# Optimization experiments

Measured on AMD Instinct MI355X. Metric: run time of the kernel, lower is better.

## Reference

```python
import jax, jax.numpy as jnp
import numpy as np

B, D, T, K = 8, 512, 2048, 8192


def setup_inputs() -> dict:
    key = jax.random.key(0)
    k1, k2 = jax.random.split(key)
    latents = jax.random.normal(k1, (B, D, T), dtype=jnp.float32)
    # nn.Embedding weight initialized uniform(-1/K, 1/K)
    embedding = jax.random.uniform(k2, (K, D), dtype=jnp.float32,
                                   minval=-1.0 / K, maxval=1.0 / K)
    return {"latents": latents, "embedding": embedding}


def reference(latents, embedding):
    # latents: [B, D, T] -> [B, T, D]
    x = jnp.transpose(latents, (0, 2, 1))
    # argmin over squared distance == argmin over cdist(p=2), so output matches torch.
    x_sq = jnp.sum(x * x, axis=-1, keepdims=True)            # [B, T, 1]
    e_sq = jnp.sum(embedding * embedding, axis=-1)           # [K]
    cross = jnp.einsum("btd,kd->btk", x, embedding)          # [B, T, K]
    dist2 = x_sq - 2.0 * cross + e_sq                        # [B, T, K]
    encoding_inds = jnp.argmin(dist2, axis=-1)               # [B, T] int
    quantized = embedding[encoding_inds]                     # [B, T, D]
    return jnp.transpose(quantized, (0, 2, 1))               # [B, D, T]
```

## Files before the change

kernel.cpp:

```cpp
#include <hip/hip_runtime.h>
#include <hip/hip_bf16.h>
#include <cstdint>

constexpr int Dv = 512;
constexpr int Tv = 2048;
constexpr int Kv = 8192;
constexpr int BT = 16384;

constexpr int BQ = 128;
constexpr int BK = 128;
constexpr int BD = 32;
constexpr int NKC = Kv / BK;
constexpr int BPQ = 6;
constexpr int NBLK = (BT / BQ) * BPQ;

__global__ void vq_xsq(const float* __restrict__ lat, float* __restrict__ xsq) {
    int q = blockIdx.x * 256 + threadIdx.x;
    int b = q >> 11, t = q & 2047;
    const float* p = lat + (size_t)b * Dv * Tv + t;
    float a = 0.f;
    #pragma unroll 8
    for (int d = 0; d < Dv; ++d) {
        float v = p[(size_t)d * Tv];
        a = fmaf(v, v, a);
    }
    xsq[q] = a;
}

__global__ void vq_esq(const float* __restrict__ emb, float* __restrict__ esq) {
    int gid = blockIdx.x * 256 + threadIdx.x;
    int k = gid >> 6;
    int l = threadIdx.x & 63;
    const float* p = emb + (size_t)k * Dv + l;
    float a = 0.f;
    #pragma unroll
    for (int i = 0; i < 8; ++i) {
        float v = p[i * 64];
        a = fmaf(v, v, a);
    }
    #pragma unroll
    for (int off = 32; off; off >>= 1) a += __shfl_down(a, off, 64);
    if (l == 0) esq[k] = a;
}

__global__ void vq_init(unsigned long long* __restrict__ keys) {
    int q = blockIdx.x * 256 + threadIdx.x;
    keys[q] = 0xFFFFFFFFFFFFFFFFull;
}

__global__ __launch_bounds__(256, 3) void vq_main(
        const float* __restrict__ lat, const float* __restrict__ emb,
        const float* __restrict__ xsq, const float* __restrict__ esq,
        unsigned long long* __restrict__ keys) {
    __shared__ float Xs[BD][BQ];
    __shared__ float Es[BD][BK];

    const int tid = threadIdx.x;
    const int bid = blockIdx.x;
    const int qb  = bid / BPQ;
    const int sub = bid - qb * BPQ;
    const int q0 = qb * BQ;
    const int b  = q0 >> 11;
    const int t0 = q0 & 2047;
    const int cnt = (sub < 4) ? 11 : 10;
    const int kc0 = (sub < 4) ? sub * 11 : 44 + (sub - 4) * 10;

    const int tx = (tid & 7) | (((tid >> 6) & 1) << 3);
    const int ty = ((tid >> 3) & 7) | (((tid >> 7) & 1) << 3);

    const int sq   = tid & 31;
    const int srow = tid >> 5;
    const int dq   = tid & 7;
    const int ekk  = tid >> 3;
    const int fsw  = dq << 2;

    float best[8];
    int   bidx[8];
    float xs[8];
    #pragma unroll
    for (int i = 0; i < 8; ++i) {
        best[i] = 3.4e38f;
        bidx[i] = 0x7fffffff;
        xs[i] = xsq[q0 + ty * 8 + i];
    }

    const float* latb = lat + (size_t)b * Dv * Tv + t0;
    float* const esw = &Es[0][0];

    for (int kc = kc0; kc < kc0 + cnt; ++kc) {
        const int k0 = kc * BK;
        float c[8][8];
        #pragma unroll
        for (int i = 0; i < 8; ++i)
            #pragma unroll
            for (int j = 0; j < 8; ++j) c[i][j] = 0.f;

        for (int dc = 0; dc < Dv / BD; ++dc) {
            const int d0 = dc * BD;
            __syncthreads();
            #pragma unroll
            for (int i = 0; i < 4; ++i) {
                int dd = srow + i * 8;
                float4 v = *(const float4*)(latb + (size_t)(d0 + dd) * Tv + sq * 4);
                *(float4*)&Xs[dd][sq * 4] = v;
            }
            #pragma unroll
            for (int i = 0; i < 4; ++i) {
                int kk = ekk + i * 32;
                float4 v = *(const float4*)(emb + (size_t)(k0 + kk) * Dv + d0 + dq * 4);
                int ksw = kk ^ fsw;
                esw[(dq * 4 + 0) * BK + ksw] = v.x;
                esw[(dq * 4 + 1) * BK + ksw] = v.y;
                esw[(dq * 4 + 2) * BK + ksw] = v.z;
                esw[(dq * 4 + 3) * BK + ksw] = v.w;
            }
            __syncthreads();

            #pragma unroll 4
            for (int dd = 0; dd < BD; ++dd) {
                const int g = (dd >> 2) << 2;
                const float4 xa = *(const float4*)&Xs[dd][ty * 8];
                const float4 xb = *(const float4*)&Xs[dd][ty * 8 + 4];
                const float4 ea = *(const float4*)&esw[dd * BK + ((tx * 8) ^ g)];
                const float4 eb = *(const float4*)&esw[dd * BK + ((tx * 8 + 4) ^ g)];
                #define VQ_ROW(i, XV)                       \
                    c[i][0] = fmaf(XV, ea.x, c[i][0]);      \
                    c[i][1] = fmaf(XV, ea.y, c[i][1]);      \
                    c[i][2] = fmaf(XV, ea.z, c[i][2]);      \
                    c[i][3] = fmaf(XV, ea.w, c[i][3]);      \
                    c[i][4] = fmaf(XV, eb.x, c[i][4]);      \
                    c[i][5] = fmaf(XV, eb.y, c[i][5]);      \
                    c[i][6] = fmaf(XV, eb.z, c[i][6]);      \
                    c[i][7] = fmaf(XV, eb.w, c[i][7]);
                VQ_ROW(0, xa.x) VQ_ROW(1, xa.y) VQ_ROW(2, xa.z) VQ_ROW(3, xa.w)
                VQ_ROW(4, xb.x) VQ_ROW(5, xb.y) VQ_ROW(6, xb.z) VQ_ROW(7, xb.w)
                #undef VQ_ROW
            }
        }

        float es8[8];
        #pragma unroll
        for (int j = 0; j < 8; ++j) es8[j] = esq[k0 + tx * 8 + j];
        #pragma unroll
        for (int i = 0; i < 8; ++i)
            #pragma unroll
            for (int j = 0; j < 8; ++j) {
                float dist = fmaf(-2.0f, c[i][j], xs[i]) + es8[j];
                int kk = k0 + tx * 8 + j;
                if (dist < best[i]) { best[i] = dist; bidx[i] = kk; }
            }
    }

    __syncthreads();
    float* redv = &Xs[0][0];
    int*   redi = (int*)&Es[0][0];
    #pragma unroll
    for (int i = 0; i < 8; ++i) {
        redv[(ty * 16 + tx) * 8 + i] = best[i];
        redi[(ty * 16 + tx) * 8 + i] = bidx[i];
    }
    __syncthreads();
    if (tid < 128) {
        int yy = tid >> 3, ii = tid & 7;
        float bv = 3.4e38f;
        int bi = 0x7fffffff;
        #pragma unroll
        for (int t = 0; t < 16; ++t) {
            float v = redv[(yy * 16 + t) * 8 + ii];
            int  ix = redi[(yy * 16 + t) * 8 + ii];
            if (v < bv || (v == bv && ix < bi)) { bv = v; bi = ix; }
        }
        int q = q0 + yy * 8 + ii;
        unsigned long long key =
            ((unsigned long long)__float_as_uint(bv) << 32) | (unsigned int)bi;
        atomicMin(&keys[q], key);
    }
}

__global__ void vq_gather(const float* __restrict__ emb,
                          const unsigned long long* __restrict__ keys,
                          float* __restrict__ out) {
    int blk = blockIdx.x;
    int tid = threadIdx.x;
    int tl = tid & 63, dg = tid >> 6;
    int q = blk * 64 + tl;
    int b = q >> 11, t = q & 2047;
    int idx = (int)(keys[q] & 0xFFFFFFFFull);
    const float* er = emb + (size_t)idx * Dv + dg * 128;
    float* ob = out + ((size_t)b * Dv + dg * 128) * Tv + t;
    #pragma unroll 8
    for (int i = 0; i < 128; ++i) ob[(size_t)i * Tv] = er[i];
}

extern "C" void kernel_launch(void* const* d_in, const int* in_sizes, int n_in,
                              void* d_out, int out_size, void* d_ws, size_t ws_size,
                              hipStream_t stream) {
    (void)in_sizes; (void)n_in; (void)out_size; (void)ws_size;
    const float* lat = (const float*)d_in[0];
    const float* emb = (const float*)d_in[1];
    float* out = (float*)d_out;

    char* ws = (char*)d_ws;
    float* xsq = (float*)(ws);
    float* esq = (float*)(ws + (64 << 10));
    unsigned long long* keys =
        (unsigned long long*)(ws + (96 << 10));

    vq_init <<<BT / 256, 256, 0, stream>>>(keys);
    vq_xsq  <<<BT / 256, 256, 0, stream>>>(lat, xsq);
    vq_esq  <<<Kv / 4,   256, 0, stream>>>(emb, esq);
    vq_main <<<NBLK, 256, 0, stream>>>(lat, emb, xsq, esq, keys);
    vq_gather<<<BT / 64, 256, 0, stream>>>(emb, keys, out);
}
```

Before: 1.874 ms.

## Add bf16 MFMA candidate filter with exact fp32 rescoring of near-minimum codes

Converts the latents (transposed) and the codebook to bf16 and computes all distances with MFMA 16x16x32 bf16 instructions. Each query keeps a running minimum, and codes within an error margin derived from the query's L1 norm are written to a candidate list. A rescore kernel then recomputes only those candidates exactly in fp32 and takes the argmin. This replaces the full fp32 FMA GEMM with tensor-core work plus a sparse exact pass, at the cost of relying on a heuristic margin, atomic contention on the candidate counter, a fixed candidate cap, and a fallback to the exact kernel when the workspace is too small.

Result: slower. 4.549 ms (+142.8%).

```diff
diff --git a/kernel.cpp b/kernel.cpp
--- a/kernel.cpp
+++ b/kernel.cpp
@@ -6,25 +6,30 @@
 constexpr int Tv = 2048;
 constexpr int Kv = 8192;
 constexpr int BT = 16384;
-
-constexpr int BQ = 128;
-constexpr int BK = 128;
-constexpr int BD = 32;
-constexpr int NKC = Kv / BK;
-constexpr int BPQ = 6;
-constexpr int NBLK = (BT / BQ) * BPQ;
-
-__global__ void vq_xsq(const float* __restrict__ lat, float* __restrict__ xsq) {
+constexpr unsigned CAP = 4u << 20;
+
+typedef __bf16 v8bf __attribute__((ext_vector_type(8)));
+typedef float  f32x4 __attribute__((ext_vector_type(4)));
+typedef unsigned long long u64;
+
+__device__ __forceinline__ float margin2(float S) {
+    return 3.9e-6f * S + 3.2e-4f;
+}
+
+__global__ void vq_xsq(const float* __restrict__ lat, float* __restrict__ xsq,
+                       float* __restrict__ Ssum) {
     int q = blockIdx.x * 256 + threadIdx.x;
     int b = q >> 11, t = q & 2047;
     const float* p = lat + (size_t)b * Dv * Tv + t;
-    float a = 0.f;
+    float a = 0.f, s = 0.f;
     #pragma unroll 8
     for (int d = 0; d < Dv; ++d) {
         float v = p[(size_t)d * Tv];
         a = fmaf(v, v, a);
+        s = s + fabsf(v);
     }
     xsq[q] = a;
+    Ssum[q] = s;
 }
 
 __global__ void vq_esq(const float* __restrict__ emb, float* __restrict__ esq) {
@@ -43,60 +48,245 @@
     if (l == 0) esq[k] = a;
 }
 
-__global__ void vq_init(unsigned long long* __restrict__ keys) {
+__global__ void vq_init_keys(u64* __restrict__ keys) {
     int q = blockIdx.x * 256 + threadIdx.x;
     keys[q] = 0xFFFFFFFFFFFFFFFFull;
 }
-
-__global__ __launch_bounds__(256, 3) void vq_main(
+__global__ void vq_init_aux(unsigned* __restrict__ qmin, unsigned* __restrict__ ctr) {
+    int q = blockIdx.x * 256 + threadIdx.x;
+    qmin[q] = 0xFFFFFFFFu;
+    if (q == 0) *ctr = 0u;
+}
+
+__global__ void vq_cvt_e(const float* __restrict__ emb, ushort* __restrict__ Ebf) {
+    int i = blockIdx.x * 256 + threadIdx.x;
+    const float4 v0 = *(const float4*)(emb + (size_t)i * 8);
+    const float4 v1 = *(const float4*)(emb + (size_t)i * 8 + 4);
+    ushort o[8];
+    float f[8] = {v0.x, v0.y, v0.z, v0.w, v1.x, v1.y, v1.z, v1.w};
+    #pragma unroll
+    for (int j = 0; j < 8; ++j) {
+        __hip_bfloat16 h = __float2bfloat16(f[j]);
+        o[j] = *(ushort*)&h;
+    }
+    *(uint4*)(Ebf + (size_t)i * 8) = *(uint4*)o;
+}
+
+__global__ void vq_cvt_x(const float* __restrict__ lat, ushort* __restrict__ Xbf) {
+    __shared__ float Xs[64][65];
+    int blk = blockIdx.x;
+    int tb = blk & 31, db = (blk >> 5) & 7, b = blk >> 8;
+    int d0 = db * 64, t0 = tb * 64;
+    int tid = threadIdx.x;
+    #pragma unroll
+    for (int i = 0; i < 4; ++i) {
+        int r = (tid >> 4) + i * 16;
+        int c = (tid & 15) * 4;
+        float4 v = *(const float4*)(lat + ((size_t)(b * Dv + d0 + r)) * Tv + t0 + c);
+        Xs[r][c] = v.x; Xs[r][c + 1] = v.y; Xs[r][c + 2] = v.z; Xs[r][c + 3] = v.w;
+    }
+    __syncthreads();
+    int tt = tid >> 2, dg = tid & 3;
+    int q = b * Tv + t0 + tt;
+    #pragma unroll
+    for (int i = 0; i < 2; ++i) {
+        ushort o[8];
+        #pragma unroll
+        for (int j = 0; j < 8; ++j) {
+            __hip_bfloat16 h = __float2bfloat16(Xs[dg * 16 + i * 8 + j][tt]);
+            o[j] = *(ushort*)&h;
+        }
+        *(uint4*)(Xbf + (size_t)q * Dv + d0 + dg * 16 + i * 8) = *(uint4*)o;
+    }
+}
+
+__global__ void vq_mfma(const ushort* __restrict__ Xbf, const ushort* __restrict__ Ebf,
+                        const float* __restrict__ es, const float* __restrict__ Ssum,
+                        unsigned* __restrict__ qmin, u64* __restrict__ cand,
+                        unsigned* __restrict__ ctr) {
+    __shared__ ushort Abuf[128 * 40];
+    __shared__ ushort Bbuf[128 * 40];
+    __shared__ unsigned tminl[128];
+    __shared__ float thrl[128];
+
+    const int tid = threadIdx.x;
+    const int bid = blockIdx.x;
+    const int q0 = (bid >> 6) * 128;
+    const int k0 = (bid & 63) * 128;
+    const int w = tid >> 6, l = tid & 63;
+    const int wr = w >> 1, wc = w & 1;
+
+    const int ar = tid >> 1, ah = tid & 1;
+
+    f32x4 acc[4][4] = {};
+
+    const ushort* Ag = Xbf + (size_t)(q0 + ar) * Dv + ah * 16;
+    const ushort* Bg = Ebf + (size_t)(k0 + ar) * Dv + ah * 16;
+
+    uint4 pa0 = *(const uint4*)(Ag);
+    uint4 pa1 = *(const uint4*)(Ag + 8);
+    uint4 pb0 = *(const uint4*)(Bg);
+    uint4 pb1 = *(const uint4*)(Bg + 8);
+
+    for (int s = 0; s < 16; ++s) {
+        __syncthreads();
+        *(uint4*)&Abuf[ar * 40 + ah * 16] = pa0;
+        *(uint4*)&Abuf[ar * 40 + ah * 16 + 8] = pa1;
+        *(uint4*)&Bbuf[ar * 40 + ah * 16] = pb0;
+        *(uint4*)&Bbuf[ar * 40 + ah * 16 + 8] = pb1;
+        __syncthreads();
+        if (s < 15) {
+            int d0 = (s + 1) * 32;
+            pa0 = *(const uint4*)(Ag + d0);
+            pa1 = *(const uint4*)(Ag + d0 + 8);
+            pb0 = *(const uint4*)(Bg + d0);
+            pb1 = *(const uint4*)(Bg + d0 + 8);
+        }
+        v8bf afr[4], bfc[4];
+        #pragma unroll
+        for (int f = 0; f < 4; ++f) {
+            int arow = wr * 64 + f * 16 + (l & 15);
+            afr[f] = __builtin_bit_cast(v8bf, *(const uint4*)&Abuf[arow * 40 + (l >> 4) * 8]);
+            int brow = wc * 64 + f * 16 + (l & 15);
+            bfc[f] = __builtin_bit_cast(v8bf, *(const uint4*)&Bbuf[brow * 40 + (l >> 4) * 8]);
+        }
+        #pragma unroll
+        for (int fr = 0; fr < 4; ++fr)
+            #pragma unroll
+            for (int fc = 0; fc < 4; ++fc)
+                acc[fr][fc] = __builtin_amdgcn_mfma_f32_16x16x32_bf16(
+                    afr[fr], bfc[fc], acc[fr][fc], 0, 0, 0);
+    }
+
+    if (tid < 128) tminl[tid] = 0xFFFFFFFFu;
+    __syncthreads();
+
+    float esv[4];
+    #pragma unroll
+    for (int fc = 0; fc < 4; ++fc) esv[fc] = es[k0 + wc * 64 + fc * 16 + (l & 15)];
+
+    #pragma unroll
+    for (int fr = 0; fr < 4; ++fr) {
+        float rmin[4] = {3.4e38f, 3.4e38f, 3.4e38f, 3.4e38f};
+        #pragma unroll
+        for (int fc = 0; fc < 4; ++fc)
+            #pragma unroll
+            for (int v = 0; v < 4; ++v) {
+                float kf = fmaf(-2.0f, acc[fr][fc][v], esv[fc]) + 1.0f;
+                rmin[v] = fminf(rmin[v], kf);
+            }
+        #pragma unroll
+        for (int v = 0; v < 4; ++v) {
+            float m = rmin[v];
+            m = fminf(m, __shfl_xor(m, 1, 64));
+            m = fminf(m, __shfl_xor(m, 2, 64));
+            m = fminf(m, __shfl_xor(m, 4, 64));
+            m = fminf(m, __shfl_xor(m, 8, 64));
+            if ((l & 15) == 0)
+                atomicMin(&tminl[wr * 64 + fr * 16 + (l >> 4) * 4 + v], __float_as_uint(m));
+        }
+    }
+    __syncthreads();
+    if (tid < 128) {
+        unsigned tm = tminl[tid];
+        unsigned old = atomicMin(&qmin[q0 + tid], tm);
+        unsigned eff = old < tm ? old : tm;
+        thrl[tid] = __uint_as_float(eff) + margin2(Ssum[q0 + tid]);
+    }
+    __syncthreads();
+    #pragma unroll
+    for (int fr = 0; fr < 4; ++fr)
+        #pragma unroll
+        for (int fc = 0; fc < 4; ++fc)
+            #pragma unroll
+            for (int v = 0; v < 4; ++v) {
+                float kf = fmaf(-2.0f, acc[fr][fc][v], esv[fc]) + 1.0f;
+                int qloc = wr * 64 + fr * 16 + (l >> 4) * 4 + v;
+                if (kf <= thrl[qloc]) {
+                    unsigned id = atomicAdd(ctr, 1u);
+                    if (id < CAP) {
+                        int kk = k0 + wc * 64 + fc * 16 + (l & 15);
+                        cand[id] = ((u64)__float_as_uint(kf) << 32)
+                                 | ((u64)(unsigned)(q0 + qloc) << 13) | (unsigned)kk;
+                    }
+                }
+            }
+}
+
+__global__ void vq_rescore(const float* __restrict__ lat, const float* __restrict__ emb,
+                           const float* __restrict__ xs, const float* __restrict__ es,
+                           const float* __restrict__ Ssum,
+                           const unsigned* __restrict__ qmin,
+                           const u64* __restrict__ cand, const unsigned* __restrict__ ctr,
+                           u64* __restrict__ keys) {
+    unsigned total = *ctr;
+    if (total > CAP) total = CAP;
+    for (unsigned i = blockIdx.x * 256 + threadIdx.x; i < total; i += 4096 * 256) {
+        u64 c = cand[i];
+        float kf = __uint_as_float((unsigned)(c >> 32));
+        int q = (int)((c >> 13) & 16383u);
+        int k = (int)(c & 8191u);
+        float thr = __uint_as_float(qmin[q]) + margin2(Ssum[q]);
+        if (kf > thr) continue;
+        int b = q >> 11, t = q & 2047;
+        const float* xr = lat + (size_t)b * Dv * Tv + t;
+        const float* er = emb + (size_t)k * Dv;
+        float cc = 0.f;
+        #pragma unroll 8
+        for (int d = 0; d < Dv; ++d)
+            cc = fmaf(xr[(size_t)d * Tv], er[d], cc);
+        float dist = fmaf(-2.0f, cc, xs[q]) + es[k];
+        u64 key = ((u64)__float_as_uint(dist) << 32) | (unsigned)k;
+        atomicMin(&keys[q], key);
+    }
+}
+
+__global__ void vq_gather(const float* __restrict__ emb, const u64* __restrict__ keys,
+                          float* __restrict__ out) {
+    int blk = blockIdx.x;
+    int tid = threadIdx.x;
+    int tl = tid & 63, dg = tid >> 6;
+    int q = blk * 64 + tl;
+    int b = q >> 11, t = q & 2047;
+    int idx = (int)(keys[q] & 0xFFFFFFFFull);
+    const float* er = emb + (size_t)idx * Dv + dg * 128;
+    float* ob = out + ((size_t)b * Dv + dg * 128) * Tv + t;
+    #pragma unroll 8
+    for (int i = 0; i < 128; ++i) ob[(size_t)i * Tv] = er[i];
+}
+
+constexpr int FBQ = 128, FBK = 128, FBD = 32, FBPQ = 6;
+__global__ __launch_bounds__(256, 3) void vq_main_exact(
         const float* __restrict__ lat, const float* __restrict__ emb,
         const float* __restrict__ xsq, const float* __restrict__ esq,
-        unsigned long long* __restrict__ keys) {
-    __shared__ float Xs[BD][BQ];
-    __shared__ float Es[BD][BK];
-
-    const int tid = threadIdx.x;
-    const int bid = blockIdx.x;
-    const int qb  = bid / BPQ;
-    const int sub = bid - qb * BPQ;
-    const int q0 = qb * BQ;
-    const int b  = q0 >> 11;
-    const int t0 = q0 & 2047;
+        u64* __restrict__ keys) {
+    __shared__ float Xs[FBD][FBQ];
+    __shared__ float Es[FBD][FBK];
+    const int tid = threadIdx.x, bid = blockIdx.x;
+    const int qb = bid / FBPQ, sub = bid - qb * FBPQ;
+    const int q0 = qb * FBQ, b = q0 >> 11, t0 = q0 & 2047;
     const int cnt = (sub < 4) ? 11 : 10;
     const int kc0 = (sub < 4) ? sub * 11 : 44 + (sub - 4) * 10;
-
     const int tx = (tid & 7) | (((tid >> 6) & 1) << 3);
     const int ty = ((tid >> 3) & 7) | (((tid >> 7) & 1) << 3);
-
-    const int sq   = tid & 31;
-    const int srow = tid >> 5;
-    const int dq   = tid & 7;
-    const int ekk  = tid >> 3;
-    const int fsw  = dq << 2;
-
-    float best[8];
-    int   bidx[8];
-    float xs[8];
+    const int sq = tid & 31, srow = tid >> 5;
+    const int dq = tid & 7, ekk = tid >> 3, fsw = dq << 2;
+    float best[8]; int bidx[8]; float xsv[8];
     #pragma unroll
     for (int i = 0; i < 8; ++i) {
-        best[i] = 3.4e38f;
-        bidx[i] = 0x7fffffff;
-        xs[i] = xsq[q0 + ty * 8 + i];
-    }
-
+        best[i] = 3.4e38f; bidx[i] = 0x7fffffff; xsv[i] = xsq[q0 + ty * 8 + i];
+    }
     const float* latb = lat + (size_t)b * Dv * Tv + t0;
     float* const esw = &Es[0][0];
-
     for (int kc = kc0; kc < kc0 + cnt; ++kc) {
-        const int k0 = kc * BK;
+        const int k0 = kc * FBK;
         float c[8][8];
         #pragma unroll
         for (int i = 0; i < 8; ++i)
             #pragma unroll
             for (int j = 0; j < 8; ++j) c[i][j] = 0.f;
-
-        for (int dc = 0; dc < Dv / BD; ++dc) {
-            const int d0 = dc * BD;
+        for (int dc = 0; dc < Dv / FBD; ++dc) {
+            const int d0 = dc * FBD;
             __syncthreads();
             #pragma unroll
             for (int i = 0; i < 4; ++i) {
@@ -109,20 +299,19 @@
                 int kk = ekk + i * 32;
                 float4 v = *(const float4*)(emb + (size_t)(k0 + kk) * Dv + d0 + dq * 4);
                 int ksw = kk ^ fsw;
-                esw[(dq * 4 + 0) * BK + ksw] = v.x;
-                esw[(dq * 4 + 1) * BK + ksw] = v.y;
-                esw[(dq * 4 + 2) * BK + ksw] = v.z;
-                esw[(dq * 4 + 3) * BK + ksw] = v.w;
+                esw[(dq * 4 + 0) * FBK + ksw] = v.x;
+                esw[(dq * 4 + 1) * FBK + ksw] = v.y;
+                esw[(dq * 4 + 2) * FBK + ksw] = v.z;
+                esw[(dq * 4 + 3) * FBK + ksw] = v.w;
             }
             __syncthreads();
-
             #pragma unroll 4
-            for (int dd = 0; dd < BD; ++dd) {
+            for (int dd = 0; dd < FBD; ++dd) {
                 const int g = (dd >> 2) << 2;
                 const float4 xa = *(const float4*)&Xs[dd][ty * 8];
                 const float4 xb = *(const float4*)&Xs[dd][ty * 8 + 4];
-                const float4 ea = *(const float4*)&esw[dd * BK + ((tx * 8) ^ g)];
-                const float4 eb = *(const float4*)&esw[dd * BK + ((tx * 8 + 4) ^ g)];
+                const float4 ea = *(const float4*)&esw[dd * FBK + ((tx * 8) ^ g)];
+                const float4 eb = *(const float4*)&esw[dd * FBK + ((tx * 8 + 4) ^ g)];
                 #define VQ_ROW(i, XV)                       \
                     c[i][0] = fmaf(XV, ea.x, c[i][0]);      \
                     c[i][1] = fmaf(XV, ea.y, c[i][1]);      \
@@ -137,7 +326,6 @@
                 #undef VQ_ROW
             }
         }
-
         float es8[8];
         #pragma unroll
         for (int j = 0; j < 8; ++j) es8[j] = esq[k0 + tx * 8 + j];
@@ -145,15 +333,14 @@
         for (int i = 0; i < 8; ++i)
             #pragma unroll
             for (int j = 0; j < 8; ++j) {
-                float dist = fmaf(-2.0f, c[i][j], xs[i]) + es8[j];
+                float dist = fmaf(-2.0f, c[i][j], xsv[i]) + es8[j];
                 int kk = k0 + tx * 8 + j;
                 if (dist < best[i]) { best[i] = dist; bidx[i] = kk; }
             }
     }
-
     __syncthreads();
     float* redv = &Xs[0][0];
-    int*   redi = (int*)&Es[0][0];
+    int* redi = (int*)&Es[0][0];
     #pragma unroll
     for (int i = 0; i < 8; ++i) {
         redv[(ty * 16 + tx) * 8 + i] = best[i];
@@ -162,53 +349,51 @@
     __syncthreads();
     if (tid < 128) {
         int yy = tid >> 3, ii = tid & 7;
-        float bv = 3.4e38f;
-        int bi = 0x7fffffff;
+        float bv = 3.4e38f; int bi = 0x7fffffff;
         #pragma unroll
         for (int t = 0; t < 16; ++t) {
             float v = redv[(yy * 16 + t) * 8 + ii];
-            int  ix = redi[(yy * 16 + t) * 8 + ii];
+            int ix = redi[(yy * 16 + t) * 8 + ii];
             if (v < bv || (v == bv && ix < bi)) { bv = v; bi = ix; }
         }
         int q = q0 + yy * 8 + ii;
-        unsigned long long key =
-            ((unsigned long long)__float_as_uint(bv) << 32) | (unsigned int)bi;
+        u64 key = ((u64)__float_as_uint(bv) << 32) | (unsigned)bi;
         atomicMin(&keys[q], key);
     }
-}
-
-__global__ void vq_gather(const float* __restrict__ emb,
-                          const unsigned long long* __restrict__ keys,
-                          float* __restrict__ out) {
-    int blk = blockIdx.x;
-    int tid = threadIdx.x;
-    int tl = tid & 63, dg = tid >> 6;
-    int q = blk * 64 + tl;
-    int b = q >> 11, t = q & 2047;
-    int idx = (int)(keys[q] & 0xFFFFFFFFull);
-    const float* er = emb + (size_t)idx * Dv + dg * 128;
-    float* ob = out + ((size_t)b * Dv + dg * 128) * Tv + t;
-    #pragma unroll 8
-    for (int i = 0; i < 128; ++i) ob[(size_t)i * Tv] = er[i];
 }
 
 extern "C" void kernel_launch(void* const* d_in, const int* in_sizes, int n_in,
                               void* d_out, int out_size, void* d_ws, size_t ws_size,
                               hipStream_t stream) {
-    (void)in_sizes; (void)n_in; (void)out_size; (void)ws_size;
+    (void)in_sizes; (void)n_in; (void)out_size;
     const float* lat = (const float*)d_in[0];
     const float* emb = (const float*)d_in[1];
     float* out = (float*)d_out;
 
     char* ws = (char*)d_ws;
-    float* xsq = (float*)(ws);
-    float* esq = (float*)(ws + (64 << 10));
-    unsigned long long* keys =
-        (unsigned long long*)(ws + (96 << 10));
-
-    vq_init <<<BT / 256, 256, 0, stream>>>(keys);
-    vq_xsq  <<<BT / 256, 256, 0, stream>>>(lat, xsq);
-    vq_esq  <<<Kv / 4,   256, 0, stream>>>(emb, esq);
-    vq_main <<<NBLK, 256, 0, stream>>>(lat, emb, xsq, esq, keys);
+    float*    xs   = (float*)(ws);
+    float*    Ssum = (float*)(ws + (64 << 10));
+    float*    es   = (float*)(ws + (128 << 10));
+    unsigned* qmin = (unsigned*)(ws + (160 << 10));
+    u64*      keys = (u64*)(ws + (224 << 10));
+    unsigned* ctr  = (unsigned*)(ws + (352 << 10));
+    u64*      cand = (u64*)(ws + (384 << 10));
+    ushort*   Xbf  = (ushort*)(ws + (384 << 10) + ((size_t)32 << 20));
+    ushort*   Ebf  = (ushort*)(ws + (384 << 10) + ((size_t)48 << 20));
+    const size_t need = ((size_t)384 << 10) + ((size_t)56 << 20) + ((size_t)1 << 20);
+
+    vq_init_keys<<<BT / 256, 256, 0, stream>>>(keys);
+    vq_xsq<<<BT / 256, 256, 0, stream>>>(lat, xs, Ssum);
+    vq_esq<<<Kv / 4, 256, 0, stream>>>(emb, es);
+
+    if (ws_size >= need) {
+        vq_init_aux<<<BT / 256, 256, 0, stream>>>(qmin, ctr);
+        vq_cvt_e<<<2048, 256, 0, stream>>>(emb, Ebf);
+        vq_cvt_x<<<2048, 256, 0, stream>>>(lat, Xbf);
+        vq_mfma<<<8192, 256, 0, stream>>>(Xbf, Ebf, es, Ssum, qmin, cand, ctr);
+        vq_rescore<<<4096, 256, 0, stream>>>(lat, emb, xs, es, Ssum, qmin, cand, ctr, keys);
+    } else {
+        vq_main_exact<<<(BT / FBQ) * FBPQ, 256, 0, stream>>>(lat, emb, xs, es, keys);
+    }
     vq_gather<<<BT / 64, 256, 0, stream>>>(emb, keys, out);
 }
```
